# Optimization experiments

Measured on AMD Instinct MI355X. Metric: run time of the kernel, lower is better.

Reference implementation:

```python
import jax, jax.numpy as jnp
import numpy as np

TOP_K = 8  # hardcoded default in OlmoeSparseMoeBlock

def setup_inputs() -> dict:
    key = jax.random.key(0)
    k_x, k_g, k_e = jax.random.split(key, 3)
    L, E, D = 4, 16, 2048
    x = jax.random.normal(k_x, (4, 2048, D), dtype=jnp.float32)
    # nn.Linear weight layout: [out_features, in_features]
    gate_w = jax.random.normal(k_g, (L, E, D), dtype=jnp.float32) * 0.02      # gate: [E, D] per layer
    expert_w = jax.random.normal(k_e, (L, E, D, D), dtype=jnp.float32) * 0.02  # experts: [D, D] per layer/expert
    return {"x": x, "gate_w": gate_w, "expert_w": expert_w}

def _moe_block(hf, gw, ew):
    # hf: [T, D], gw: [E, D], ew: [E, D, D]
    T, D = hf.shape
    E = gw.shape[0]
    logits = hf @ gw.T                              # [T, E]
    w = jax.nn.softmax(logits, axis=-1)
    vals, idx = jax.lax.top_k(w, TOP_K)             # [T, K]
    # scatter top-k weights back to dense [T, E] routing matrix
    w_dense = jnp.zeros_like(w).at[jnp.arange(T)[:, None], idx].add(vals)
    out = jnp.zeros_like(hf)
    for e in range(E):  # small fixed expert count; each iter is a big GEMM
        out = out + w_dense[:, e:e + 1] * (hf @ ew[e].T)
    return out

def reference(x, gate_w, expert_w):
    b, t, d = x.shape
    L = gate_w.shape[0]
    h = x
    for l in range(L):
        hf = h.reshape(-1, d)
        h = _moe_block(hf, gate_w[l], expert_w[l]).reshape(b, t, d)
    return h
```

## Files before the change

### kernel.cpp

```cpp
#include <hip/hip_runtime.h>
#include <stdint.h>

#define T_TOK 8192
#define DIM   2048
#define NEXP  16
#define NLAY  4
#define TOPK  8

#define BM 128
#define BN 256
#define BK 32
#define NT 64

typedef _Float16 f16;
typedef f16   f16x8 __attribute__((ext_vector_type(8)));
typedef f16   f16x4 __attribute__((ext_vector_type(4)));
typedef float f32x4 __attribute__((ext_vector_type(4)));
typedef float fv4   __attribute__((ext_vector_type(4)));

__global__ __launch_bounds__(256) void route_kernel(
    const float* __restrict__ h, const float* __restrict__ gw,
    int* __restrict__ cnt, int* __restrict__ tok, float* __restrict__ wt)
{
  int gid  = blockIdx.x * 256 + threadIdx.x;
  int t    = gid >> 6;
  int lane = threadIdx.x & 63;
  if (t >= T_TOK) return;
  const float* hr = h + (size_t)t * DIM;
  float hreg[32];
#pragma unroll
  for (int j = 0; j < 32; ++j) hreg[j] = hr[lane + 64 * j];
  float p[16];
#pragma unroll
  for (int e = 0; e < 16; ++e) {
    const float* gr = gw + e * DIM;
    float s = 0.f;
#pragma unroll
    for (int j = 0; j < 32; ++j) s += hreg[j] * gr[lane + 64 * j];
#pragma unroll
    for (int off = 32; off; off >>= 1) s += __shfl_xor(s, off);
    p[e] = s;
  }
  float mx = p[0];
#pragma unroll
  for (int e = 1; e < 16; ++e) mx = fmaxf(mx, p[e]);
  float sum = 0.f;
#pragma unroll
  for (int e = 0; e < 16; ++e) { p[e] = expf(p[e] - mx); sum += p[e]; }
  float inv = 1.f / sum;
#pragma unroll
  for (int e = 0; e < 16; ++e) p[e] *= inv;
  if (lane < 16) {
    float mine = p[lane];
    int rank = 0;
#pragma unroll
    for (int j = 0; j < 16; ++j)
      rank += (p[j] > mine) || (p[j] == mine && j < lane);
    if (rank < TOPK) {
      int pos = atomicAdd(&cnt[lane], 1);
      tok[lane * T_TOK + pos] = t;
      wt [lane * T_TOK + pos] = mine;
    }
  }
}

__global__ __launch_bounds__(256) void split_kernel(
    const float* __restrict__ src, f16* __restrict__ hi, f16* __restrict__ lo, int n4)
{
  int i0 = blockIdx.x * 256 + threadIdx.x;
  int stride = gridDim.x * 256;
  for (int i = i0; i < n4; i += stride) {
    fv4 v = ((const fv4*)src)[i];
    f16x4 h4, l4;
#pragma unroll
    for (int j = 0; j < 4; ++j) {
      float x = v[j] * 64.f;
      f16 hh = (f16)x;
      h4[j] = hh;
      l4[j] = (f16)(x - (float)hh);
    }
    ((f16x4*)hi)[i] = h4;
    ((f16x4*)lo)[i] = l4;
  }
}

__global__ __launch_bounds__(256) void wsplit_kernel(
    const float* __restrict__ src, f16* __restrict__ hi, f16* __restrict__ lo)
{
  const int eidx = blockIdx.z;
  const int r0   = blockIdx.y * 32;
  const int k0   = blockIdx.x * 64;
  __shared__ f16 th[32 * 9 * 8];
  __shared__ f16 tl[32 * 9 * 8];
  const int rr = threadIdx.x >> 3, c8 = threadIdx.x & 7;
  const float* s = src + ((size_t)eidx * DIM + r0 + rr) * DIM + k0 + c8 * 8;
  fv4 v0 = *(const fv4*)s;
  fv4 v1 = *(const fv4*)(s + 4);
  f16x8 hv, lv;
#pragma unroll
  for (int j = 0; j < 4; ++j) {
    float x = v0[j] * 64.f; f16 hh = (f16)x; hv[j] = hh; lv[j] = (f16)(x - (float)hh);
    float y = v1[j] * 64.f; f16 h2 = (f16)y; hv[4 + j] = h2; lv[4 + j] = (f16)(y - (float)h2);
  }
  *(f16x8*)&th[(rr * 9 + c8) * 8] = hv;
  *(f16x8*)&tl[(rr * 9 + c8) * 8] = lv;
  __syncthreads();
  const int c8w = threadIdx.x >> 5, rw = threadIdx.x & 31;
  f16x8 oh = *(const f16x8*)&th[(rw * 9 + c8w) * 8];
  f16x8 ol = *(const f16x8*)&tl[(rw * 9 + c8w) * 8];
  size_t o = (((size_t)eidx * (DIM / 8) + (k0 / 8 + c8w)) * DIM + r0 + rw) * 8;
  *(f16x8*)&hi[o] = oh;
  *(f16x8*)&lo[o] = ol;
}

__global__ __launch_bounds__(256, 2) void moe_gemm(
    const f16* __restrict__ A1, const f16* __restrict__ A2,
    const f16* __restrict__ W1t, const f16* __restrict__ W2t,
    const int* __restrict__ tok, const float* __restrict__ wt,
    const int* __restrict__ cnt, float* __restrict__ out)
{
  const int b  = blockIdx.x;
  const int w  = (b >> 9) * 8 + (b & 7);
  const int my = (b >> 3) & 63;
  const int e  = w >> 3;
  const int ce = cnt[e];
  const int m0 = my * BM;
  if (m0 >= ce) return;
  const int n0 = (w & 7) * BN;

  __shared__ f16 lsA1[BM * BK];
  __shared__ f16 lsA2[BM * BK];
  __shared__ f16 lsW1[2][BN * BK];
  __shared__ f16 lsW2[2][BN * BK];

  const int tid = threadIdx.x;

  const int ar0 = tid >> 2;
  const int gc  = (tid & 3) ^ ((ar0 >> 1) & 3);
  const size_t aofs0 = (size_t)tok[e * T_TOK + min(m0 + ar0,      ce - 1)] * DIM + gc * 8;
  const size_t aofs1 = (size_t)tok[e * T_TOK + min(m0 + ar0 + 64, ce - 1)] * DIM + gc * 8;
  const size_t wbase = (size_t)e * (DIM / 8) * DIM * 8 + ((size_t)n0 + tid) * 8;

  auto stageA = [&](int kt) {
    const int k0 = kt * BK;
    __builtin_amdgcn_global_load_lds(
        (const __attribute__((address_space(1))) void*)(A1 + aofs0 + k0),
        (__attribute__((address_space(3))) void*)(&lsA1[tid * 8]), 16, 0, 0);
    __builtin_amdgcn_global_load_lds(
        (const __attribute__((address_space(1))) void*)(A1 + aofs1 + k0),
        (__attribute__((address_space(3))) void*)(&lsA1[(tid + 256) * 8]), 16, 0, 0);
    __builtin_amdgcn_global_load_lds(
        (const __attribute__((address_space(1))) void*)(A2 + aofs0 + k0),
        (__attribute__((address_space(3))) void*)(&lsA2[tid * 8]), 16, 0, 0);
    __builtin_amdgcn_global_load_lds(
        (const __attribute__((address_space(1))) void*)(A2 + aofs1 + k0),
        (__attribute__((address_space(3))) void*)(&lsA2[(tid + 256) * 8]), 16, 0, 0);
  };
  auto stageW = [&](int kt, int bb) {
    const int kc0 = kt * 4;
#pragma unroll
    for (int j = 0; j < 4; ++j) {
      __builtin_amdgcn_global_load_lds(
          (const __attribute__((address_space(1))) void*)(W1t + wbase + (size_t)(kc0 + j) * DIM * 8),
          (__attribute__((address_space(3))) void*)(&lsW1[bb][(tid + 256 * j) * 8]), 16, 0, 0);
      __builtin_amdgcn_global_load_lds(
          (const __attribute__((address_space(1))) void*)(W2t + wbase + (size_t)(kc0 + j) * DIM * 8),
          (__attribute__((address_space(3))) void*)(&lsW2[bb][(tid + 256 * j) * 8]), 16, 0, 0);
    }
  };

  const int lane = tid & 63;
  const int wid  = tid >> 6;
  const int wm   = wid & 1;
  const int wn   = wid >> 1;
  const int lr   = lane & 15;
  const int lk   = lane >> 4;
  const int aswz = lk ^ ((lr >> 1) & 3);

  f32x4 acc[4][8];
#pragma unroll
  for (int i = 0; i < 4; ++i)
#pragma unroll
    for (int j = 0; j < 8; ++j)
      acc[i][j] = (f32x4){0.f, 0.f, 0.f, 0.f};

  stageA(0);
  stageW(0, 0);
  asm volatile("s_waitcnt vmcnt(0)" ::: "memory");
  __builtin_amdgcn_s_barrier();
  __builtin_amdgcn_sched_barrier(0);

  int cur = 0;
  for (int kt = 0; kt < NT; ++kt) {
    const bool pf = (kt + 1 < NT);
    f16x8 a1F[4], a2F[4], w1F[8], w2F[8];

#pragma unroll
    for (int mi = 0; mi < 4; ++mi) {
      int r = wm * 64 + mi * 16 + lr;
      a1F[mi] = *(const f16x8*)&lsA1[r * 32 + aswz * 8];
      a2F[mi] = *(const f16x8*)&lsA2[r * 32 + aswz * 8];
    }
#pragma unroll
    for (int ni = 0; ni < 8; ++ni) {
      int r = wn * 128 + ni * 16 + lr;
      w1F[ni] = *(const f16x8*)&lsW1[cur][lk * 2048 + r * 8];
    }
    asm volatile("s_waitcnt lgkmcnt(0)" ::: "memory");
    __builtin_amdgcn_sched_barrier(0);
    __builtin_amdgcn_s_barrier();
    __builtin_amdgcn_sched_barrier(0);
    if (pf) { stageA(kt + 1); stageW(kt + 1, cur ^ 1); }

#pragma unroll
    for (int ni = 0; ni < 8; ++ni) {
      int r = wn * 128 + ni * 16 + lr;
      w2F[ni] = *(const f16x8*)&lsW2[cur][lk * 2048 + r * 8];
    }

    __builtin_amdgcn_s_setprio(1);
#pragma unroll
    for (int mi = 0; mi < 4; ++mi)
#pragma unroll
      for (int ni = 0; ni < 8; ++ni)
        acc[mi][ni] = __builtin_amdgcn_mfma_f32_16x16x32_f16(a1F[mi], w1F[ni], acc[mi][ni], 0, 0, 0);
#pragma unroll
    for (int mi = 0; mi < 4; ++mi)
#pragma unroll
      for (int ni = 0; ni < 8; ++ni)
        acc[mi][ni] = __builtin_amdgcn_mfma_f32_16x16x32_f16(a2F[mi], w1F[ni], acc[mi][ni], 0, 0, 0);
#pragma unroll
    for (int mi = 0; mi < 4; ++mi)
#pragma unroll
      for (int ni = 0; ni < 8; ++ni)
        acc[mi][ni] = __builtin_amdgcn_mfma_f32_16x16x32_f16(a1F[mi], w2F[ni], acc[mi][ni], 0, 0, 0);
    __builtin_amdgcn_s_setprio(0);

    if (pf) {
      asm volatile("s_waitcnt vmcnt(0)" ::: "memory");
      __builtin_amdgcn_s_barrier();
      __builtin_amdgcn_sched_barrier(0);
    }
    cur ^= 1;
  }

  const int ebase = e * T_TOK;
#pragma unroll
  for (int mi = 0; mi < 4; ++mi) {
#pragma unroll
    for (int q = 0; q < 4; ++q) {
      int pos = m0 + wm * 64 + mi * 16 + lk * 4 + q;
      if (pos < ce) {
        int tt = tok[ebase + pos];
        float sc = wt[ebase + pos] * (1.0f / 4096.0f);
        float* orow = out + (size_t)tt * DIM + n0 + wn * 128;
#pragma unroll
        for (int ni = 0; ni < 8; ++ni)
          atomicAdd(&orow[ni * 16 + lr], sc * acc[mi][ni][q]);
      }
    }
  }
}

extern "C" void kernel_launch(void* const* d_in, const int* in_sizes, int n_in,
                              void* d_out, int out_size, void* d_ws, size_t ws_size,
                              hipStream_t stream) {
  const float* x  = (const float*)d_in[0];
  const float* gw = (const float*)d_in[1];
  const float* ew = (const float*)d_in[2];
  float* out = (float*)d_out;

  char* ws = (char*)d_ws;
  float* hA  = (float*)ws;
  f16*   A1  = (f16*)(ws + 67108864ull);
  f16*   A2  = (f16*)(ws + 100663296ull);
  f16*   W1t = (f16*)(ws + 134217728ull);
  f16*   W2t = (f16*)(ws + 268435456ull);
  int*   tok = (int*)(ws + 402653184ull);
  float* wt  = (float*)(ws + 403177472ull);
  int*   cnt = (int*)(ws + 403701760ull);

  const float* hin = x;
  float* houts[4] = {hA, out, hA, out};
  for (int l = 0; l < NLAY; ++l) {
    float* hout = houts[l];
    hipMemsetAsync(cnt, 0, 64, stream);
    route_kernel<<<T_TOK / 4, 256, 0, stream>>>(hin, gw + (size_t)l * NEXP * DIM, cnt, tok, wt);
    split_kernel<<<4096, 256, 0, stream>>>(hin, A1, A2, T_TOK * DIM / 4);
    {
      dim3 gt(DIM / 64, DIM / 32, NEXP);
      wsplit_kernel<<<gt, 256, 0, stream>>>(ew + (size_t)l * NEXP * DIM * DIM, W1t, W2t);
    }
    hipMemsetAsync(hout, 0, (size_t)T_TOK * DIM * 4, stream);
    moe_gemm<<<16 * 64 * 8, 256, 0, stream>>>(A1, A2, W1t, W2t, tok, wt, cnt, hout);
    hin = hout;
  }
}
```

Baseline: 7.059 ms.

## Load gathered activation fragments directly from global into registers, bypassing LDS

Removes the LDS staging buffers for the two gathered activation operands. Each lane now computes per-row gathered byte offsets once and loads its f16x8 fragments straight from global memory every K step. Only the weight tiles stay double-buffered through LDS. One in-loop barrier is dropped and replaced by a partial vmcnt wait, which cuts LDS traffic and synchronisation. The cost is that activation loads are issued in the same iteration that consumes them, so their global latency is not hidden by prefetch, and waves sharing rows now fetch the same data redundantly.

```diff
diff --git a/kernel.cpp b/kernel.cpp
--- a/kernel.cpp
+++ b/kernel.cpp
@@ -128,34 +128,13 @@
   if (m0 >= ce) return;
   const int n0 = (w & 7) * BN;
 
-  __shared__ f16 lsA1[BM * BK];
-  __shared__ f16 lsA2[BM * BK];
   __shared__ f16 lsW1[2][BN * BK];
   __shared__ f16 lsW2[2][BN * BK];
 
   const int tid = threadIdx.x;
 
-  const int ar0 = tid >> 2;
-  const int gc  = (tid & 3) ^ ((ar0 >> 1) & 3);
-  const size_t aofs0 = (size_t)tok[e * T_TOK + min(m0 + ar0,      ce - 1)] * DIM + gc * 8;
-  const size_t aofs1 = (size_t)tok[e * T_TOK + min(m0 + ar0 + 64, ce - 1)] * DIM + gc * 8;
   const size_t wbase = (size_t)e * (DIM / 8) * DIM * 8 + ((size_t)n0 + tid) * 8;
 
-  auto stageA = [&](int kt) {
-    const int k0 = kt * BK;
-    __builtin_amdgcn_global_load_lds(
-        (const __attribute__((address_space(1))) void*)(A1 + aofs0 + k0),
-        (__attribute__((address_space(3))) void*)(&lsA1[tid * 8]), 16, 0, 0);
-    __builtin_amdgcn_global_load_lds(
-        (const __attribute__((address_space(1))) void*)(A1 + aofs1 + k0),
-        (__attribute__((address_space(3))) void*)(&lsA1[(tid + 256) * 8]), 16, 0, 0);
-    __builtin_amdgcn_global_load_lds(
-        (const __attribute__((address_space(1))) void*)(A2 + aofs0 + k0),
-        (__attribute__((address_space(3))) void*)(&lsA2[tid * 8]), 16, 0, 0);
-    __builtin_amdgcn_global_load_lds(
-        (const __attribute__((address_space(1))) void*)(A2 + aofs1 + k0),
-        (__attribute__((address_space(3))) void*)(&lsA2[(tid + 256) * 8]), 16, 0, 0);
-  };
   auto stageW = [&](int kt, int bb) {
     const int kc0 = kt * 4;
 #pragma unroll
@@ -175,7 +154,16 @@
   const int wn   = wid >> 1;
   const int lr   = lane & 15;
   const int lk   = lane >> 4;
-  const int aswz = lk ^ ((lr >> 1) & 3);
+
+  uint32_t voff[4];
+#pragma unroll
+  for (int mi = 0; mi < 4; ++mi) {
+    int row = wm * 64 + mi * 16 + lr;
+    int pos = min(m0 + row, ce - 1);
+    voff[mi] = (uint32_t)tok[e * T_TOK + pos] * (DIM * 2) + lk * 16;
+  }
+  const char* A1b = (const char*)A1;
+  const char* A2b = (const char*)A2;
 
   f32x4 acc[4][8];
 #pragma unroll
@@ -184,7 +172,6 @@
     for (int j = 0; j < 8; ++j)
       acc[i][j] = (f32x4){0.f, 0.f, 0.f, 0.f};
 
-  stageA(0);
   stageW(0, 0);
   asm volatile("s_waitcnt vmcnt(0)" ::: "memory");
   __builtin_amdgcn_s_barrier();
@@ -193,30 +180,27 @@
   int cur = 0;
   for (int kt = 0; kt < NT; ++kt) {
     const bool pf = (kt + 1 < NT);
+    const int kb = kt * 64;
     f16x8 a1F[4], a2F[4], w1F[8], w2F[8];
 
 #pragma unroll
-    for (int mi = 0; mi < 4; ++mi) {
-      int r = wm * 64 + mi * 16 + lr;
-      a1F[mi] = *(const f16x8*)&lsA1[r * 32 + aswz * 8];
-      a2F[mi] = *(const f16x8*)&lsA2[r * 32 + aswz * 8];
-    }
+    for (int mi = 0; mi < 4; ++mi)
+      a1F[mi] = *(const f16x8*)(A1b + voff[mi] + kb);
+#pragma unroll
+    for (int mi = 0; mi < 4; ++mi)
+      a2F[mi] = *(const f16x8*)(A2b + voff[mi] + kb);
+    if (pf) stageW(kt + 1, cur ^ 1);
+
 #pragma unroll
     for (int ni = 0; ni < 8; ++ni) {
-      int r = wn * 128 + ni * 16 + lr;
-      w1F[ni] = *(const f16x8*)&lsW1[cur][lk * 2048 + r * 8];
+      int off = (lk * 256 + wn * 128 + ni * 16 + lr) * 8;
+      w1F[ni] = *(const f16x8*)&lsW1[cur][off];
+      w2F[ni] = *(const f16x8*)&lsW2[cur][off];
     }
     asm volatile("s_waitcnt lgkmcnt(0)" ::: "memory");
+    if (pf) asm volatile("s_waitcnt vmcnt(8)" ::: "memory");
+    else    asm volatile("s_waitcnt vmcnt(0)" ::: "memory");
     __builtin_amdgcn_sched_barrier(0);
-    __builtin_amdgcn_s_barrier();
-    __builtin_amdgcn_sched_barrier(0);
-    if (pf) { stageA(kt + 1); stageW(kt + 1, cur ^ 1); }
-
-#pragma unroll
-    for (int ni = 0; ni < 8; ++ni) {
-      int r = wn * 128 + ni * 16 + lr;
-      w2F[ni] = *(const f16x8*)&lsW2[cur][lk * 2048 + r * 8];
-    }
 
     __builtin_amdgcn_s_setprio(1);
 #pragma unroll
```

Result: slower. 7.668 ms (+8.6%).
